# Optimization experiments

Measured on AMD Instinct MI355X. Metric: run time of the kernel, lower is better.

Reference implementation:

```python
import jax, jax.numpy as jnp
import numpy as np

N_EMBD = 1024
N_HEAD = 16
HEAD_SIZE = 64


def setup_inputs() -> dict:
    key = jax.random.key(0)
    ks = jax.random.split(key, 6)
    B, T, C, H, D = 2, 2048, N_EMBD, N_HEAD, HEAD_SIZE
    s = 1.0 / np.sqrt(C)
    x = jax.random.normal(ks[0], (B, T, C), dtype=jnp.float32)
    Wq = jax.random.normal(ks[1], (H, C, D), dtype=jnp.float32) * s
    Wk = jax.random.normal(ks[2], (H, C, D), dtype=jnp.float32) * s
    Wv = jax.random.normal(ks[3], (H, C, D), dtype=jnp.float32) * s
    Wo = jax.random.normal(ks[4], (H * D, C), dtype=jnp.float32) * (1.0 / np.sqrt(H * D))
    bo = jax.random.normal(ks[5], (C,), dtype=jnp.float32) * 0.01
    return {"x": x, "Wq": Wq, "Wk": Wk, "Wv": Wv, "Wo": Wo, "bo": bo}


def reference(x, Wq, Wk, Wv, Wo, bo):
    B, T, C = x.shape
    H, _, D = Wq.shape
    # Per-head projections, batched across heads: [B,H,T,D]
    q = jnp.einsum('btc,hcd->bhtd', x, Wq)
    k = jnp.einsum('btc,hcd->bhtd', x, Wk)
    v = jnp.einsum('btc,hcd->bhtd', x, Wv)
    # NOTE: original scales by sqrt(C) = sqrt(n_embd), not sqrt(head_size)
    scale = 1.0 / jnp.sqrt(jnp.float32(C))
    att = jnp.einsum('bhtd,bhsd->bhts', q, k) * scale  # [B,H,T,T]
    causal = jnp.tril(jnp.ones((T, T), dtype=bool))
    att = jnp.where(causal, att, -jnp.inf)
    att = jax.nn.softmax(att, axis=-1)
    # dropout omitted (eval mode / deterministic reference)
    out = jnp.einsum('bhts,bhsd->bhtd', att, v)  # [B,H,T,D]
    out = out.transpose(0, 2, 1, 3).reshape(B, T, H * D)
    return out @ Wo + bo
```

## Files before the change

kernel.cpp:

```cpp
#include <hip/hip_runtime.h>
#include <hip/hip_bf16.h>


typedef __hip_bfloat16 bf16;
typedef __bf16 v8bf __attribute__((ext_vector_type(8)));
typedef float  v4f  __attribute__((ext_vector_type(4)));
typedef unsigned long long u64;
typedef unsigned int u32;

#define MFMA16(a, b, c) __builtin_amdgcn_mfma_f32_16x16x32_bf16((a), (b), (c), 0, 0, 0)

__device__ __forceinline__ bf16 f2b(float x) { return __float2bfloat16(x); }
__device__ __forceinline__ __bf16 f2braw(float x) {
  bf16 t = __float2bfloat16(x);
  return *reinterpret_cast<__bf16*>(&t);
}
__device__ __forceinline__ unsigned short f2bu(float x) {
  bf16 t = __float2bfloat16(x);
  return *reinterpret_cast<unsigned short*>(&t);
}

__device__ __forceinline__ void load16_lds(const bf16* gptr, const bf16* lptr) {
  __builtin_amdgcn_global_load_lds(
      (const __attribute__((address_space(1))) u32*)gptr,
      (__attribute__((address_space(3))) u32*)lptr, 16, 0, 0);
}

__global__ __launch_bounds__(256) void cvt_x_kernel(
    const float* __restrict__ x, bf16* __restrict__ xb)
{
  size_t i = ((size_t)blockIdx.x * 256 + threadIdx.x) * 8;
  float4 f0 = *(const float4*)(x + i);
  float4 f1 = *(const float4*)(x + i + 4);
  v8bf v;
  v[0] = f2braw(f0.x); v[1] = f2braw(f0.y); v[2] = f2braw(f0.z); v[3] = f2braw(f0.w);
  v[4] = f2braw(f1.x); v[5] = f2braw(f1.y); v[6] = f2braw(f1.z); v[7] = f2braw(f1.w);
  *(v8bf*)(xb + i) = v;
}

__global__ __launch_bounds__(256) void transpose_kernel(
    const float* __restrict__ in, bf16* __restrict__ outp,
    int R, int Cc, size_t in_zstride, size_t out_zstride)
{
  __shared__ float Lt[32][33];
  const float* ib = in + (size_t)blockIdx.z * in_zstride;
  bf16* ob = outp + (size_t)blockIdx.z * out_zstride;
  const int j0 = blockIdx.x * 32;
  const int i0 = blockIdx.y * 32;
  const int tx = threadIdx.x & 31, ty = threadIdx.x >> 5;
  #pragma unroll
  for (int r = 0; r < 4; ++r)
    Lt[ty + 8 * r][tx] = ib[(size_t)(i0 + ty + 8 * r) * Cc + j0 + tx];
  __syncthreads();
  #pragma unroll
  for (int r = 0; r < 4; ++r)
    ob[(size_t)(j0 + ty + 8 * r) * R + i0 + tx] = f2b(Lt[tx][ty + 8 * r]);
}

__global__ __launch_bounds__(256) void qkv_gemm_kernel(
    const bf16* __restrict__ xb, const bf16* __restrict__ wt,
    bf16* __restrict__ qkv)
{
  __shared__ __align__(16) bf16 Ash[128][32];
  __shared__ __align__(16) bf16 Bsh[128][32];

  const int mt = blockIdx.x, nt = blockIdx.y;
  const int tid = threadIdx.x, w = tid >> 6, lane = tid & 63;
  const int ln = lane & 15, quad = lane >> 4;
  const int wm = w >> 1, wn = w & 1;
  const int m0 = mt * 128, n0 = nt * 128;

  const v4f vzero = {0.f, 0.f, 0.f, 0.f};
  v4f acc[4][4];
  #pragma unroll
  for (int mf = 0; mf < 4; ++mf)
    #pragma unroll
    for (int nf = 0; nf < 4; ++nf) acc[mf][nf] = vzero;

  const int srow = lane >> 2, sseg = (lane & 3) * 8;
  const bf16* ga = xb + (size_t)(m0 + 32 * w + srow) * 1024 + sseg;
  const bf16* gb = wt + (size_t)(n0 + 32 * w + srow) * 1024 + sseg;

  for (int k0 = 0; k0 < 1024; k0 += 32) {
    __syncthreads();
    load16_lds(ga + k0,             &Ash[32 * w][0]);
    load16_lds(ga + 16 * 1024 + k0, &Ash[32 * w + 16][0]);
    load16_lds(gb + k0,             &Bsh[32 * w][0]);
    load16_lds(gb + 16 * 1024 + k0, &Bsh[32 * w + 16][0]);
    __syncthreads();

    v8bf af[4], bfv[4];
    #pragma unroll
    for (int mf = 0; mf < 4; ++mf)
      af[mf] = *(const v8bf*)&Ash[wm * 64 + mf * 16 + ln][quad * 8];
    #pragma unroll
    for (int nf = 0; nf < 4; ++nf)
      bfv[nf] = *(const v8bf*)&Bsh[wn * 64 + nf * 16 + ln][quad * 8];
    #pragma unroll
    for (int mf = 0; mf < 4; ++mf)
      #pragma unroll
      for (int nf = 0; nf < 4; ++nf)
        acc[mf][nf] = MFMA16(af[mf], bfv[nf], acc[mf][nf]);
  }

  const int jcol0 = n0 + wn * 64;
  const int p = jcol0 >> 10;
  const int h = (jcol0 >> 6) & 15;
  const float scale = (p == 0) ? 0.03125f : 1.0f;

  if (p < 2) {
    bf16* base = qkv + (size_t)p * 4194304 + (size_t)h * 262144;
    #pragma unroll
    for (int mf = 0; mf < 4; ++mf)
      #pragma unroll
      for (int nf = 0; nf < 4; ++nf) {
        int d = nf * 16 + ln;
        #pragma unroll
        for (int r = 0; r < 4; ++r) {
          int m = m0 + wm * 64 + mf * 16 + quad * 4 + r;
          base[(size_t)m * 64 + d] = f2b(acc[mf][nf][r] * scale);
        }
      }
  } else {
    bf16* vb = qkv + (size_t)2 * 4194304 + (size_t)h * 262144;
    #pragma unroll
    for (int mf = 0; mf < 4; ++mf) {
      int mrow = m0 + wm * 64 + mf * 16 + quad * 4;
      int bi = mrow >> 11, t0 = mrow & 2047;
      #pragma unroll
      for (int nf = 0; nf < 4; ++nf) {
        int d = nf * 16 + ln;
        u64 pk = (u64)f2bu(acc[mf][nf][0]) |
                 ((u64)f2bu(acc[mf][nf][1]) << 16) |
                 ((u64)f2bu(acc[mf][nf][2]) << 32) |
                 ((u64)f2bu(acc[mf][nf][3]) << 48);
        *(u64*)(vb + (size_t)bi * 131072 + (size_t)d * 2048 + t0) = pk;
      }
    }
  }
}

__global__ __launch_bounds__(256) void attn_kernel(
    const bf16* __restrict__ qkv, bf16* __restrict__ att)
{
  __shared__ __align__(16) bf16 Ksh[64][64];
  __shared__ __align__(16) bf16 Vsh[64][64];
  __shared__ __align__(16) __bf16 Psh[4][16][72];

  const int fid = blockIdx.x;
  const int lo = fid & 255, hi = fid >> 8;
  const int mt = hi ? (15 - (lo & 15)) : (lo & 15);
  const int b = hi, h = (lo >> 4) & 15;
  const int row0 = mt * 128;

  const int tid = threadIdx.x, w = tid >> 6, lane = tid & 63;
  const int ln = lane & 15, quad = lane >> 4;

  const bf16* qbase  = qkv + (size_t)h * 262144 + (size_t)b * 131072;
  const bf16* kbase  = qbase + 4194304;
  const bf16* vtbase = qbase + 8388608;

  v8bf aq[2][2];
  #pragma unroll
  for (int mc = 0; mc < 2; ++mc)
    #pragma unroll
    for (int ks = 0; ks < 2; ++ks)
      aq[mc][ks] = *(const v8bf*)(qbase +
          (size_t)(row0 + w * 32 + mc * 16 + ln) * 64 + ks * 32 + quad * 8);

  v8bf vone;
  {
    unsigned short u = 0x3F80;
    __bf16 one_e = *reinterpret_cast<__bf16*>(&u);
    #pragma unroll
    for (int j = 0; j < 8; ++j) vone[j] = one_e;
  }

  const v4f vzero = {0.f, 0.f, 0.f, 0.f};
  v4f o[2][4], lacc[2];
  #pragma unroll
  for (int mc = 0; mc < 2; ++mc) {
    lacc[mc] = vzero;
    #pragma unroll
    for (int n = 0; n < 4; ++n) o[mc][n] = vzero;
  }

  const float NEG = -30000.0f;
  const int wrow = row0 + w * 32;
  const int wk_last = (wrow + 31) >> 6;
  const int kb_end = (row0 + 127) >> 6;

  for (int kb = 0; kb <= kb_end; ++kb) {
    __syncthreads();
    {
      const bf16* gk = kbase + (size_t)(kb * 64 + w * 16 + (lane >> 3)) * 64 +
                       (lane & 7) * 8;
      load16_lds(gk,          &Ksh[w * 16][0]);
      load16_lds(gk + 8 * 64, &Ksh[w * 16 + 8][0]);
      const bf16* gv = vtbase + (size_t)(w * 16 + (lane >> 3)) * 2048 +
                       kb * 64 + (lane & 7) * 8;
      load16_lds(gv,            &Vsh[w * 16][0]);
      load16_lds(gv + 8 * 2048, &Vsh[w * 16 + 8][0]);
    }
    __syncthreads();

    if (kb <= wk_last) {
      v8bf kf[2][4], vf[2][4];
      #pragma unroll
      for (int ks = 0; ks < 2; ++ks)
        #pragma unroll
        for (int nf = 0; nf < 4; ++nf) {
          kf[ks][nf] = *(const v8bf*)&Ksh[nf * 16 + ln][ks * 32 + quad * 8];
          vf[ks][nf] = *(const v8bf*)&Vsh[nf * 16 + ln][ks * 32 + quad * 8];
        }

      #pragma unroll
      for (int mc = 0; mc < 2; ++mc) {
        v4f s[4];
        #pragma unroll
        for (int nf = 0; nf < 4; ++nf) s[nf] = vzero;
        #pragma unroll
        for (int ks = 0; ks < 2; ++ks)
          #pragma unroll
          for (int nf = 0; nf < 4; ++nf)
            s[nf] = MFMA16(aq[mc][ks], kf[ks][nf], s[nf]);

        if (kb == wk_last) {
          int row = wrow + mc * 16 + quad * 4;
          #pragma unroll
          for (int nf = 0; nf < 4; ++nf) {
            int col = kb * 64 + nf * 16 + ln;
            #pragma unroll
            for (int r = 0; r < 4; ++r)
              if (col > row + r) s[nf][r] = NEG;
          }
        }

        #pragma unroll
        for (int nf = 0; nf < 4; ++nf)
          #pragma unroll
          for (int r = 0; r < 4; ++r)
            Psh[w][quad * 4 + r][nf * 16 + ln] = f2braw(__expf(s[nf][r]));
        __asm__ volatile("s_waitcnt lgkmcnt(0)" ::: "memory");

        #pragma unroll
        for (int ks = 0; ks < 2; ++ks) {
          v8bf pf = *(const v8bf*)&Psh[w][ln][ks * 32 + quad * 8];
          lacc[mc] = MFMA16(pf, vone, lacc[mc]);
          #pragma unroll
          for (int nf = 0; nf < 4; ++nf)
            o[mc][nf] = MFMA16(pf, vf[ks][nf], o[mc][nf]);
        }
      }
    }
  }

  #pragma unroll
  for (int mc = 0; mc < 2; ++mc) {
    v4f inv;
    #pragma unroll
    for (int r = 0; r < 4; ++r) inv[r] = 1.0f / lacc[mc][r];
    #pragma unroll
    for (int nf = 0; nf < 4; ++nf)
      #pragma unroll
      for (int r = 0; r < 4; ++r) {
        int m = b * 2048 + wrow + mc * 16 + quad * 4 + r;
        att[(size_t)m * 1024 + h * 64 + nf * 16 + ln] = f2b(o[mc][nf][r] * inv[r]);
      }
  }
}

__global__ __launch_bounds__(256) void out_gemm_kernel(
    const bf16* __restrict__ att, const bf16* __restrict__ wot,
    const float* __restrict__ bo, float* __restrict__ out)
{
  __shared__ __align__(16) bf16 Ash[128][32];
  __shared__ __align__(16) bf16 Bsh[64][32];

  const int mt = blockIdx.x, nt = blockIdx.y;
  const int tid = threadIdx.x, w = tid >> 6, lane = tid & 63;
  const int ln = lane & 15, quad = lane >> 4;
  const int wm = w >> 1, wn = w & 1;
  const int m0 = mt * 128, n0 = nt * 64;

  const v4f vzero = {0.f, 0.f, 0.f, 0.f};
  v4f acc[4][2];
  #pragma unroll
  for (int mf = 0; mf < 4; ++mf)
    #pragma unroll
    for (int nf = 0; nf < 2; ++nf) acc[mf][nf] = vzero;

  const int srow = lane >> 2, sseg = (lane & 3) * 8;
  const bf16* ga = att + (size_t)(m0 + 32 * w + srow) * 1024 + sseg;
  const bf16* gb = wot + (size_t)(n0 + 16 * w + srow) * 1024 + sseg;

  for (int k0 = 0; k0 < 1024; k0 += 32) {
    __syncthreads();
    load16_lds(ga + k0,             &Ash[32 * w][0]);
    load16_lds(ga + 16 * 1024 + k0, &Ash[32 * w + 16][0]);
    load16_lds(gb + k0,             &Bsh[16 * w][0]);
    __syncthreads();

    v8bf af[4], bfv[2];
    #pragma unroll
    for (int mf = 0; mf < 4; ++mf)
      af[mf] = *(const v8bf*)&Ash[wm * 64 + mf * 16 + ln][quad * 8];
    #pragma unroll
    for (int nf = 0; nf < 2; ++nf)
      bfv[nf] = *(const v8bf*)&Bsh[wn * 32 + nf * 16 + ln][quad * 8];
    #pragma unroll
    for (int mf = 0; mf < 4; ++mf)
      #pragma unroll
      for (int nf = 0; nf < 2; ++nf)
        acc[mf][nf] = MFMA16(af[mf], bfv[nf], acc[mf][nf]);
  }

  #pragma unroll
  for (int nf = 0; nf < 2; ++nf) {
    int j = n0 + wn * 32 + nf * 16 + ln;
    float bias = bo[j];
    #pragma unroll
    for (int mf = 0; mf < 4; ++mf)
      #pragma unroll
      for (int r = 0; r < 4; ++r) {
        int m = m0 + wm * 64 + mf * 16 + quad * 4 + r;
        out[(size_t)m * 1024 + j] = acc[mf][nf][r] + bias;
      }
  }
}

extern "C" void kernel_launch(void* const* d_in, const int* in_sizes, int n_in,
                              void* d_out, int out_size, void* d_ws, size_t ws_size,
                              hipStream_t stream) {
  const float* x  = (const float*)d_in[0];
  const float* Wq = (const float*)d_in[1];
  const float* Wk = (const float*)d_in[2];
  const float* Wv = (const float*)d_in[3];
  const float* Wo = (const float*)d_in[4];
  const float* bo = (const float*)d_in[5];
  float* out = (float*)d_out;

  bf16* xb  = (bf16*)d_ws;
  bf16* wt  = xb + 4194304;
  bf16* wot = xb + 7340032;
  bf16* qkv = xb + 8388608;
  bf16* att = xb + 20971520;

  cvt_x_kernel<<<2048, 256, 0, stream>>>(x, xb);
  transpose_kernel<<<dim3(2, 32, 16), 256, 0, stream>>>(Wq, wt,           1024, 64, 65536, 65536);
  transpose_kernel<<<dim3(2, 32, 16), 256, 0, stream>>>(Wk, wt + 1048576, 1024, 64, 65536, 65536);
  transpose_kernel<<<dim3(2, 32, 16), 256, 0, stream>>>(Wv, wt + 2097152, 1024, 64, 65536, 65536);
  transpose_kernel<<<dim3(32, 32, 1), 256, 0, stream>>>(Wo, wot, 1024, 1024, 0, 0);

  qkv_gemm_kernel<<<dim3(32, 24), 256, 0, stream>>>(xb, wt, qkv);
  attn_kernel<<<512, 256, 0, stream>>>(qkv, att);
  out_gemm_kernel<<<dim3(32, 16), 256, 0, stream>>>(att, wot, bo, out);
}
```

Before: 199.3 us.

## Split attention K/V LDS tiles into half-width buffers and merge QKV weight transposes

The attention kernel now stores the K and V tiles as two 64x32 halves instead of one 64x64 array. Each row is 64 bytes, so the 16-byte fragment reads from the MFMA k-slices map onto different LDS banks, which should reduce bank conflicts. The global-to-LDS loads are restructured to fill the two halves. The three Q/K/V weight transpose launches are merged into one grid of 48 z-slices, with a specialised Wo transpose, to cut launch overhead.

```diff
diff --git a/kernel.cpp b/kernel.cpp
--- a/kernel.cpp
+++ b/kernel.cpp
@@ -38,23 +38,40 @@
   *(v8bf*)(xb + i) = v;
 }
 
-__global__ __launch_bounds__(256) void transpose_kernel(
-    const float* __restrict__ in, bf16* __restrict__ outp,
-    int R, int Cc, size_t in_zstride, size_t out_zstride)
+__global__ __launch_bounds__(256) void transpose_qkv_kernel(
+    const float* __restrict__ Wq, const float* __restrict__ Wk,
+    const float* __restrict__ Wv, bf16* __restrict__ wt)
 {
   __shared__ float Lt[32][33];
-  const float* ib = in + (size_t)blockIdx.z * in_zstride;
-  bf16* ob = outp + (size_t)blockIdx.z * out_zstride;
+  const int z = blockIdx.z, p = z >> 4, h = z & 15;
+  const float* ib = ((p == 0) ? Wq : (p == 1) ? Wk : Wv) + (size_t)h * 65536;
+  bf16* ob = wt + (size_t)z * 65536;
   const int j0 = blockIdx.x * 32;
   const int i0 = blockIdx.y * 32;
   const int tx = threadIdx.x & 31, ty = threadIdx.x >> 5;
   #pragma unroll
   for (int r = 0; r < 4; ++r)
-    Lt[ty + 8 * r][tx] = ib[(size_t)(i0 + ty + 8 * r) * Cc + j0 + tx];
+    Lt[ty + 8 * r][tx] = ib[(size_t)(i0 + ty + 8 * r) * 64 + j0 + tx];
   __syncthreads();
   #pragma unroll
   for (int r = 0; r < 4; ++r)
-    ob[(size_t)(j0 + ty + 8 * r) * R + i0 + tx] = f2b(Lt[tx][ty + 8 * r]);
+    ob[(size_t)(j0 + ty + 8 * r) * 1024 + i0 + tx] = f2b(Lt[tx][ty + 8 * r]);
+}
+
+__global__ __launch_bounds__(256) void transpose_wo_kernel(
+    const float* __restrict__ in, bf16* __restrict__ outp)
+{
+  __shared__ float Lt[32][33];
+  const int j0 = blockIdx.x * 32;
+  const int i0 = blockIdx.y * 32;
+  const int tx = threadIdx.x & 31, ty = threadIdx.x >> 5;
+  #pragma unroll
+  for (int r = 0; r < 4; ++r)
+    Lt[ty + 8 * r][tx] = in[(size_t)(i0 + ty + 8 * r) * 1024 + j0 + tx];
+  __syncthreads();
+  #pragma unroll
+  for (int r = 0; r < 4; ++r)
+    outp[(size_t)(j0 + ty + 8 * r) * 1024 + i0 + tx] = f2b(Lt[tx][ty + 8 * r]);
 }
 
 __global__ __launch_bounds__(256) void qkv_gemm_kernel(
@@ -143,8 +160,8 @@
 __global__ __launch_bounds__(256) void attn_kernel(
     const bf16* __restrict__ qkv, bf16* __restrict__ att)
 {
-  __shared__ __align__(16) bf16 Ksh[64][64];
-  __shared__ __align__(16) bf16 Vsh[64][64];
+  __shared__ __align__(16) bf16 Ksh0[64][32], Ksh1[64][32];
+  __shared__ __align__(16) bf16 Vsh0[64][32], Vsh1[64][32];
   __shared__ __align__(16) __bf16 Psh[4][16][72];
 
   const int fid = blockIdx.x;
@@ -190,29 +207,29 @@
   const int wk_last = (wrow + 31) >> 6;
   const int kb_end = (row0 + 127) >> 6;
 
+  const int srow = lane >> 2, sseg = (lane & 3) * 8;
+
   for (int kb = 0; kb <= kb_end; ++kb) {
     __syncthreads();
     {
-      const bf16* gk = kbase + (size_t)(kb * 64 + w * 16 + (lane >> 3)) * 64 +
-                       (lane & 7) * 8;
-      load16_lds(gk,          &Ksh[w * 16][0]);
-      load16_lds(gk + 8 * 64, &Ksh[w * 16 + 8][0]);
-      const bf16* gv = vtbase + (size_t)(w * 16 + (lane >> 3)) * 2048 +
-                       kb * 64 + (lane & 7) * 8;
-      load16_lds(gv,            &Vsh[w * 16][0]);
-      load16_lds(gv + 8 * 2048, &Vsh[w * 16 + 8][0]);
+      const bf16* gk = kbase + (size_t)(kb * 64 + w * 16 + srow) * 64 + sseg;
+      load16_lds(gk,      &Ksh0[w * 16][0]);
+      load16_lds(gk + 32, &Ksh1[w * 16][0]);
+      const bf16* gv = vtbase + (size_t)(w * 16 + srow) * 2048 + kb * 64 + sseg;
+      load16_lds(gv,      &Vsh0[w * 16][0]);
+      load16_lds(gv + 32, &Vsh1[w * 16][0]);
     }
     __syncthreads();
 
     if (kb <= wk_last) {
       v8bf kf[2][4], vf[2][4];
       #pragma unroll
-      for (int ks = 0; ks < 2; ++ks)
-        #pragma unroll
-        for (int nf = 0; nf < 4; ++nf) {
-          kf[ks][nf] = *(const v8bf*)&Ksh[nf * 16 + ln][ks * 32 + quad * 8];
-          vf[ks][nf] = *(const v8bf*)&Vsh[nf * 16 + ln][ks * 32 + quad * 8];
-        }
+      for (int nf = 0; nf < 4; ++nf) {
+        kf[0][nf] = *(const v8bf*)&Ksh0[nf * 16 + ln][quad * 8];
+        kf[1][nf] = *(const v8bf*)&Ksh1[nf * 16 + ln][quad * 8];
+        vf[0][nf] = *(const v8bf*)&Vsh0[nf * 16 + ln][quad * 8];
+        vf[1][nf] = *(const v8bf*)&Vsh1[nf * 16 + ln][quad * 8];
+      }
 
       #pragma unroll
       for (int mc = 0; mc < 2; ++mc) {
@@ -347,10 +364,8 @@
   bf16* att = xb + 20971520;
 
   cvt_x_kernel<<<2048, 256, 0, stream>>>(x, xb);
-  transpose_kernel<<<dim3(2, 32, 16), 256, 0, stream>>>(Wq, wt,           1024, 64, 65536, 65536);
-  transpose_kernel<<<dim3(2, 32, 16), 256, 0, stream>>>(Wk, wt + 1048576, 1024, 64, 65536, 65536);
-  transpose_kernel<<<dim3(2, 32, 16), 256, 0, stream>>>(Wv, wt + 2097152, 1024, 64, 65536, 65536);
-  transpose_kernel<<<dim3(32, 32, 1), 256, 0, stream>>>(Wo, wot, 1024, 1024, 0, 0);
+  transpose_qkv_kernel<<<dim3(2, 32, 48), 256, 0, stream>>>(Wq, Wk, Wv, wt);
+  transpose_wo_kernel<<<dim3(32, 32), 256, 0, stream>>>(Wo, wot);
 
   qkv_gemm_kernel<<<dim3(32, 24), 256, 0, stream>>>(xb, wt, qkv);
   attn_kernel<<<512, 256, 0, stream>>>(qkv, att);
```

New measurement: 192.2 us. 1.04x faster.
